# Optimization experiments

Hardware: AMD Instinct MI355X
Metric: run time of the kernel (lower is better)

Reference implementation:

```python
import jax, jax.numpy as jnp
import numpy as np

COMMITMENT_COST = 0.25


def setup_inputs() -> dict:
    key = jax.random.key(0)
    k1, k2 = jax.random.split(key)
    x = jax.random.normal(k1, (32, 1024, 512), dtype=jnp.float32)
    codebook = jax.random.normal(k2, (8192, 512), dtype=jnp.float32)
    return {"x": x, "codebook": codebook}


def reference(x, codebook):
    D = codebook.shape[1]
    flat = x.reshape(-1, D)                                   # [N, D]
    # squared L2 distances: ||f||^2 + ||c||^2 - 2 f c^T
    distances = (
        jnp.sum(flat * flat, axis=1, keepdims=True)
        + jnp.sum(codebook * codebook, axis=1)
        - 2.0 * jnp.matmul(flat, codebook.T)                   # [N, K]
    )
    encoding_indices = jnp.argmin(distances, axis=1)           # [N]
    quantized = codebook[encoding_indices].reshape(x.shape)    # [.., D]
    commitment_loss = COMMITMENT_COST * jnp.mean(
        (jax.lax.stop_gradient(quantized) - x) ** 2
    )
    # straight-through estimator
    quantized_st = x + jax.lax.stop_gradient(quantized - x)
    return (quantized_st, commitment_loss)
```

## Files before the change

### kernel.cpp

```cpp
#include <hip/hip_runtime.h>
#include <stdint.h>

#define N_TOT 32768
#define DDIM  512
#define KCB   8192
#define NSPLIT 4
#define COLS_SPLIT (KCB / NSPLIT)
#define BN 256
#define BC 256
#define BKD 64
#define NTILES (COLS_SPLIT / BC)
#define NSTEPS (NTILES * 8)
#define MARGIN 0.15f

#define RB3 32
#define RP3 32
#define RSLOTS (RGRID3 / RP3)
#define RGRID3 2048

typedef _Float16 half8 __attribute__((ext_vector_type(8)));
typedef float    floatx4 __attribute__((ext_vector_type(4)));

typedef const __attribute__((address_space(1))) unsigned int* gas_ptr;
typedef __attribute__((address_space(3))) unsigned int* las_ptr;
__device__ __forceinline__ void gld_lds16(void* l, const void* g) {
    __builtin_amdgcn_global_load_lds((gas_ptr)g, (las_ptr)l, 16, 0, 0);
}

__device__ __forceinline__ unsigned long long shfl_xor_u64(unsigned long long v, int m) {
    unsigned int lo = (unsigned int)v, hi = (unsigned int)(v >> 32);
    lo = __shfl_xor(lo, m, 64);
    hi = __shfl_xor(hi, m, 64);
    return ((unsigned long long)hi << 32) | lo;
}

__global__ __launch_bounds__(256) void convert_x_kernel(
    const float* __restrict__ x, _Float16* __restrict__ xh) {
    size_t i = ((size_t)blockIdx.x * 256 + threadIdx.x) * 8;
    float4 v0 = *(const float4*)(x + i);
    float4 v1 = *(const float4*)(x + i + 4);
    half8 h;
    h[0] = (_Float16)v0.x; h[1] = (_Float16)v0.y; h[2] = (_Float16)v0.z; h[3] = (_Float16)v0.w;
    h[4] = (_Float16)v1.x; h[5] = (_Float16)v1.y; h[6] = (_Float16)v1.z; h[7] = (_Float16)v1.w;
    *(half8*)(xh + i) = h;
}

__global__ __launch_bounds__(256) void convert_cb_kernel(
    const float* __restrict__ cb, _Float16* __restrict__ cbh, float* __restrict__ cnorm) {
    int row = blockIdx.x * 4 + (threadIdx.x >> 6);
    int lane = threadIdx.x & 63;
    const float* src = cb + (size_t)row * DDIM + lane * 8;
    float4 v0 = *(const float4*)src;
    float4 v1 = *(const float4*)(src + 4);
    half8 h;
    h[0] = (_Float16)v0.x; h[1] = (_Float16)v0.y; h[2] = (_Float16)v0.z; h[3] = (_Float16)v0.w;
    h[4] = (_Float16)v1.x; h[5] = (_Float16)v1.y; h[6] = (_Float16)v1.z; h[7] = (_Float16)v1.w;
    *(half8*)(cbh + (size_t)row * DDIM + lane * 8) = h;
    float s = v0.x*v0.x + v0.y*v0.y + v0.z*v0.z + v0.w*v0.w
            + v1.x*v1.x + v1.y*v1.y + v1.z*v1.z + v1.w*v1.w;
#pragma unroll
    for (int off = 32; off > 0; off >>= 1) s += __shfl_down(s, off, 64);
    if (lane == 0) cnorm[row] = s;
}

__global__ __launch_bounds__(512, 2) void gemm_argmin_kernel(
    const _Float16* __restrict__ xh, const _Float16* __restrict__ cbh,
    const float* __restrict__ cnorm,
    float* __restrict__ sb1, int* __restrict__ si1, float* __restrict__ sb2) {

    __shared__ __align__(16) _Float16 smem[65536];
    char* smemb = (char*)smem;

    const int tid = threadIdx.x;
    const int wave = tid >> 6;
    const int lane = tid & 63;
    const int rowPart = wave >> 1;
    const int colPart = wave & 1;
    const int l15 = lane & 15;
    const int quad = lane >> 4;

    const int orig = blockIdx.x;
    const int wg = (orig & 7) * 64 + (orig >> 3);
    const int bx = wg & 127;
    const int by = wg >> 7;
    const int row0 = bx * BN;
    const int colBase = by * COLS_SPLIT;

    int voff[4];
#pragma unroll
    for (int r = 0; r < 4; ++r) {
        int c = wave * 256 + r * 64 + lane;
        int ar = c >> 3;
        int q  = (c & 7) ^ (ar & 7);
        voff[r] = (ar << 9) + q * 8;
    }
    const _Float16* aptr = xh + ((size_t)row0 << 9);
    const _Float16* bptr = cbh + ((size_t)colBase << 9);

    int aaddr[4], baddr[8];
#pragma unroll
    for (int i = 0; i < 4; ++i) {
        int rr = rowPart * 64 + i * 16 + l15;
        int qa = quad ^ (rr & 7);
        aaddr[i] = rr * 128 + qa * 16;
    }
#pragma unroll
    for (int j = 0; j < 8; ++j) {
        int cc = colPart * 128 + j * 16 + l15;
        int qb = quad ^ (cc & 7);
        baddr[j] = 32768 + cc * 128 + qb * 16;
    }

    float b1[16], b2[16];
    int   i1[16];
#pragma unroll
    for (int s = 0; s < 16; ++s) { b1[s] = 3.402823466e38f; b2[s] = 3.402823466e38f; i1[s] = 0; }

#define STAGE(st) do {                                                          \
        _Float16* Asb = smem + ((st) & 1) * 32768;                              \
        _Float16* Bsb = Asb + 16384;                                            \
        const int boffu = ((st) >> 3) << 17;          \
        const int d0v   = ((st) & 7) * BKD;                                     \
        _Pragma("unroll")                                                       \
        for (int r = 0; r < 4; ++r) {                                           \
            gld_lds16(Asb + (wave * 256 + r * 64) * 8,                          \
                      aptr + d0v + voff[r]);                                    \
            gld_lds16(Bsb + (wave * 256 + r * 64) * 8,                          \
                      bptr + boffu + d0v + voff[r]);                            \
        }                                                                       \
    } while (0)

    floatx4 acc[4][8];
#pragma unroll
    for (int i = 0; i < 4; ++i)
#pragma unroll
        for (int j = 0; j < 8; ++j)
            acc[i][j] = (floatx4){0.f, 0.f, 0.f, 0.f};

    STAGE(0);
    STAGE(1);

    for (int s = 0; s < NSTEPS; ++s) {
        if (s + 1 < NSTEPS) {
            asm volatile("s_waitcnt vmcnt(8)" ::: "memory");
        } else {
            asm volatile("s_waitcnt vmcnt(0)" ::: "memory");
        }
        __builtin_amdgcn_sched_barrier(0);
        __builtin_amdgcn_s_barrier();
        __builtin_amdgcn_sched_barrier(0);

        const char* Ab = smemb + (s & 1) * 65536;
        __builtin_amdgcn_s_setprio(1);
#pragma unroll
        for (int kh = 0; kh < 2; ++kh) {
            half8 af[4], bf[8];
#pragma unroll
            for (int i = 0; i < 4; ++i)
                af[i] = *(const half8*)(Ab + (aaddr[i] ^ (kh << 6)));
#pragma unroll
            for (int j = 0; j < 8; ++j)
                bf[j] = *(const half8*)(Ab + (baddr[j] ^ (kh << 6)));
#pragma unroll
            for (int i = 0; i < 4; ++i)
#pragma unroll
                for (int j = 0; j < 8; ++j)
                    acc[i][j] = __builtin_amdgcn_mfma_f32_16x16x32_f16(
                        af[i], bf[j], acc[i][j], 0, 0, 0);
        }
        __builtin_amdgcn_s_setprio(0);

        if ((s & 7) == 7) {
            const int col0 = colBase + (s >> 3) * BC;
#pragma unroll
            for (int j = 0; j < 8; ++j) {
                int col = col0 + colPart * 128 + j * 16 + l15;
                float cn = cnorm[col];
#pragma unroll
                for (int i = 0; i < 4; ++i) {
#pragma unroll
                    for (int r = 0; r < 4; ++r) {
                        float sc = fmaf(-2.0f, acc[i][j][r], cn);
                        int slot = i * 4 + r;
                        if (sc < b1[slot]) { b2[slot] = b1[slot]; b1[slot] = sc; i1[slot] = col; }
                        else if (sc < b2[slot]) b2[slot] = sc;
                    }
                }
            }
#pragma unroll
            for (int i = 0; i < 4; ++i)
#pragma unroll
                for (int j = 0; j < 8; ++j)
                    acc[i][j] = (floatx4){0.f, 0.f, 0.f, 0.f};
        }

        __builtin_amdgcn_s_barrier();
        __builtin_amdgcn_sched_barrier(0);
        if (s + 2 < NSTEPS) {
            STAGE(s + 2);
        }
    }
#undef STAGE

    __syncthreads();

#pragma unroll
    for (int m = 1; m < 16; m <<= 1) {
#pragma unroll
        for (int s = 0; s < 16; ++s) {
            float ob1 = __shfl_xor(b1[s], m, 64);
            float ob2 = __shfl_xor(b2[s], m, 64);
            int   oi1 = __shfl_xor(i1[s], m, 64);
            if (ob1 < b1[s] || (ob1 == b1[s] && oi1 < i1[s])) {
                b2[s] = fminf(b1[s], ob2);
                b1[s] = ob1; i1[s] = oi1;
            } else {
                b2[s] = fminf(b2[s], ob1);
            }
        }
    }

    float* mb1 = (float*)smem;
    float* mb2 = mb1 + 512;
    int*   mi1 = (int*)(mb2 + 512);
    if (l15 == 0) {
#pragma unroll
        for (int s = 0; s < 16; ++s) {
            int row = rowPart * 64 + (s >> 2) * 16 + quad * 4 + (s & 3);
            mb1[colPart * 256 + row] = b1[s];
            mb2[colPart * 256 + row] = b2[s];
            mi1[colPart * 256 + row] = i1[s];
        }
    }
    __syncthreads();
    if (tid < 256) {
        float a1 = mb1[tid], a2 = mb2[tid]; int ai = mi1[tid];
        float c1 = mb1[256 + tid], c2 = mb2[256 + tid]; int ci = mi1[256 + tid];
        float r1, r2; int ri;
        if (c1 < a1 || (c1 == a1 && ci < ai)) { r1 = c1; ri = ci; r2 = fminf(a1, c2); }
        else { r1 = a1; ri = ai; r2 = fminf(a2, c1); }
        size_t o = (size_t)by * N_TOT + row0 + tid;
        sb1[o] = r1; si1[o] = ri; sb2[o] = r2;
    }
}

__global__ __launch_bounds__(256) void merge_kernel(
    const float* __restrict__ sb1, const int* __restrict__ si1, const float* __restrict__ sb2,
    int* __restrict__ indices, int* __restrict__ flags,
    int* __restrict__ list, int* __restrict__ count,
    unsigned long long* __restrict__ result) {
    int n = blockIdx.x * 256 + threadIdx.x;
    float b1 = sb1[n]; int i1 = si1[n]; float b2 = sb2[n];
#pragma unroll
    for (int s = 1; s < NSPLIT; ++s) {
        float ob1 = sb1[(size_t)s * N_TOT + n];
        int   oi1 = si1[(size_t)s * N_TOT + n];
        float ob2 = sb2[(size_t)s * N_TOT + n];
        if (ob1 < b1 || (ob1 == b1 && oi1 < i1)) { b2 = fminf(b1, ob2); b1 = ob1; i1 = oi1; }
        else b2 = fminf(b2, ob1);
    }
    indices[n] = i1;
    result[n] = 0xFFFFFFFFFFFFFFFFull;
    int f = (b2 - b1 < MARGIN) ? 1 : 0;
    flags[n] = f;
    if (f) { int pos = atomicAdd(count, 1); list[pos] = n; }
}

__global__ __launch_bounds__(256) void repair3_kernel(
    const float* __restrict__ x, const float* __restrict__ cb,
    const float* __restrict__ cnorm, const int* __restrict__ list,
    const int* __restrict__ count, unsigned long long* __restrict__ result) {
    __shared__ __align__(16) float xs[RB3][512];
    __shared__ unsigned long long red[RB3][4];
    const int tid = threadIdx.x;
    const int lane = tid & 63;
    const int wv = tid >> 6;
    const int part = blockIdx.x & (RP3 - 1);
    const int slot0 = blockIdx.x >> 5;
    const int cnt = *count;
    const int nbatch = (cnt + RB3 - 1) / RB3;
    const int k = part * 256 + tid;
    const float cn = cnorm[k];
    const float* crow = cb + (size_t)k * 512;

    for (int batch = slot0; batch < nbatch; batch += RSLOTS) {
        const int rb = min(RB3, cnt - batch * RB3);
        __syncthreads();
        for (int t = tid; t < rb * 128; t += 256) {
            int b = t >> 7, d4 = t & 127;
            int n = list[batch * RB3 + b];
            ((float4*)xs[b])[d4] = ((const float4*)(x + ((size_t)n << 9)))[d4];
        }
        __syncthreads();

        float d0[RB3], d1[RB3], d2[RB3], d3[RB3];
#pragma unroll
        for (int b = 0; b < RB3; ++b) { d0[b] = 0.f; d1[b] = 0.f; d2[b] = 0.f; d3[b] = 0.f; }

        for (int t = 0; t < 512; t += 16) {
            float4 c0 = *(const float4*)(crow + t);
            float4 c1 = *(const float4*)(crow + t + 4);
            float4 c2 = *(const float4*)(crow + t + 8);
            float4 c3 = *(const float4*)(crow + t + 12);
#pragma unroll
            for (int b = 0; b < RB3; ++b) {
                float4 x0 = *(const float4*)&xs[b][t];
                float4 x1 = *(const float4*)&xs[b][t + 4];
                float4 x2 = *(const float4*)&xs[b][t + 8];
                float4 x3 = *(const float4*)&xs[b][t + 12];
                d0[b] = fmaf(c0.x, x0.x, d0[b]);  d0[b] = fmaf(c0.y, x0.y, d0[b]);
                d0[b] = fmaf(c0.z, x0.z, d0[b]);  d0[b] = fmaf(c0.w, x0.w, d0[b]);
                d1[b] = fmaf(c1.x, x1.x, d1[b]);  d1[b] = fmaf(c1.y, x1.y, d1[b]);
                d1[b] = fmaf(c1.z, x1.z, d1[b]);  d1[b] = fmaf(c1.w, x1.w, d1[b]);
                d2[b] = fmaf(c2.x, x2.x, d2[b]);  d2[b] = fmaf(c2.y, x2.y, d2[b]);
                d2[b] = fmaf(c2.z, x2.z, d2[b]);  d2[b] = fmaf(c2.w, x2.w, d2[b]);
                d3[b] = fmaf(c3.x, x3.x, d3[b]);  d3[b] = fmaf(c3.y, x3.y, d3[b]);
                d3[b] = fmaf(c3.z, x3.z, d3[b]);  d3[b] = fmaf(c3.w, x3.w, d3[b]);
            }
        }

#pragma unroll
        for (int b = 0; b < RB3; ++b) {
            float s = cn - 2.f * ((d0[b] + d1[b]) + (d2[b] + d3[b]));
            unsigned int sb = __float_as_uint(s);
            sb = (sb & 0x80000000u) ? ~sb : (sb | 0x80000000u);
            unsigned long long p = ((unsigned long long)sb << 32) | (unsigned int)k;
#pragma unroll
            for (int m = 32; m > 0; m >>= 1) {
                unsigned long long o = shfl_xor_u64(p, m);
                if (o < p) p = o;
            }
            if (lane == 0) red[b][wv] = p;
        }
        __syncthreads();
        if (tid < RB3) {
            unsigned long long p = red[tid][0];
            if (red[tid][1] < p) p = red[tid][1];
            if (red[tid][2] < p) p = red[tid][2];
            if (red[tid][3] < p) p = red[tid][3];
            if (tid < rb) {
                int n = list[batch * RB3 + tid];
                atomicMin(&result[n], p);
            }
        }
    }
}

__global__ __launch_bounds__(256) void fixup_kernel(
    const int* __restrict__ flags, const unsigned long long* __restrict__ result,
    int* __restrict__ indices) {
    int n = blockIdx.x * 256 + threadIdx.x;
    if (flags[n]) indices[n] = (int)(result[n] & 0xFFFFFFFFu);
}

__global__ void cnorm_kernel(const float* __restrict__ cb, float* __restrict__ cnorm) {
    int wave = (blockIdx.x * blockDim.x + threadIdx.x) >> 6;
    int lane = threadIdx.x & 63;
    if (wave >= KCB) return;
    const float* row = cb + (size_t)wave * DDIM;
    float s = 0.f;
#pragma unroll
    for (int j = 0; j < DDIM / 64; ++j) { float v = row[lane + 64 * j]; s += v * v; }
#pragma unroll
    for (int off = 32; off > 0; off >>= 1) s += __shfl_down(s, off, 64);
    if (lane == 0) cnorm[wave] = s;
}

#define FBN 64
#define FBD 32
#define FLDA (FBN + 4)
__global__ __launch_bounds__(256) void argmin_fp32_kernel(
    const float* __restrict__ x, const float* __restrict__ cb,
    const float* __restrict__ cnorm, int* __restrict__ indices) {
    __shared__ float As[FBD][FLDA];
    __shared__ float Bs[FBD][FLDA];
    __shared__ float redv[FBN][16];
    __shared__ int   redi[FBN][16];
    const int tid = threadIdx.x;
    const int tx = tid & 15, ty = tid >> 4;
    const int row0 = blockIdx.x * FBN;
    float best[4]; int bidx[4];
#pragma unroll
    for (int i = 0; i < 4; ++i) { best[i] = 3.402823466e+38f; bidx[i] = KCB; }
    for (int k0 = 0; k0 < KCB; k0 += 64) {
        float acc[4][4] = {};
        for (int d0 = 0; d0 < DDIM; d0 += FBD) {
#pragma unroll
            for (int t = 0; t < 2; ++t) {
                int q = tid + t * 256, rr = q >> 3, dq = q & 7;
                float4 v = *(const float4*)(x + (size_t)(row0 + rr) * DDIM + d0 + dq * 4);
                As[dq*4+0][rr] = v.x; As[dq*4+1][rr] = v.y; As[dq*4+2][rr] = v.z; As[dq*4+3][rr] = v.w;
                float4 w = *(const float4*)(cb + (size_t)(k0 + rr) * DDIM + d0 + dq * 4);
                Bs[dq*4+0][rr] = w.x; Bs[dq*4+1][rr] = w.y; Bs[dq*4+2][rr] = w.z; Bs[dq*4+3][rr] = w.w;
            }
            __syncthreads();
#pragma unroll
            for (int d = 0; d < FBD; ++d) {
                float4 av = *(const float4*)&As[d][ty * 4];
                float4 bv = *(const float4*)&Bs[d][tx * 4];
                float a[4] = {av.x, av.y, av.z, av.w}, b[4] = {bv.x, bv.y, bv.z, bv.w};
#pragma unroll
                for (int i = 0; i < 4; ++i)
#pragma unroll
                    for (int j = 0; j < 4; ++j) acc[i][j] += a[i] * b[j];
            }
            __syncthreads();
        }
#pragma unroll
        for (int j = 0; j < 4; ++j) {
            int k = k0 + tx * 4 + j;
            float cn = cnorm[k];
#pragma unroll
            for (int i = 0; i < 4; ++i) {
                float s = cn - 2.0f * acc[i][j];
                if (s < best[i] || (s == best[i] && k < bidx[i])) { best[i] = s; bidx[i] = k; }
            }
        }
    }
#pragma unroll
    for (int i = 0; i < 4; ++i) { redv[ty*4+i][tx] = best[i]; redi[ty*4+i][tx] = bidx[i]; }
    __syncthreads();
    if (tid < FBN) {
        float bv = redv[tid][0]; int bi = redi[tid][0];
#pragma unroll
        for (int t = 1; t < 16; ++t) {
            float v = redv[tid][t]; int ii = redi[tid][t];
            if (v < bv || (v == bv && ii < bi)) { bv = v; bi = ii; }
        }
        indices[row0 + tid] = bi;
    }
}

__global__ __launch_bounds__(256) void output_kernel(
    const float* __restrict__ x, const float* __restrict__ cb,
    const int* __restrict__ indices, float* __restrict__ out,
    float* __restrict__ loss_acc) {
    size_t base = ((size_t)blockIdx.x * blockDim.x + threadIdx.x) * 16;
    int n = (int)(base >> 9);
    int d = (int)(base & 511);
    int idx = indices[n];
    const float* cr = cb + (size_t)idx * DDIM + d;
    const float* xr = x + base;
    float* orow = out + base;
    float lsum = 0.f;
#pragma unroll
    for (int t = 0; t < 4; ++t) {
        float4 q  = *(const float4*)(cr + t * 4);
        float4 xv = *(const float4*)(xr + t * 4);
        float dx0 = q.x - xv.x, dx1 = q.y - xv.y, dx2 = q.z - xv.z, dx3 = q.w - xv.w;
        float4 o;
        o.x = xv.x + dx0; o.y = xv.y + dx1; o.z = xv.z + dx2; o.w = xv.w + dx3;
        *(float4*)(orow + t * 4) = o;
        lsum += dx0*dx0 + dx1*dx1 + dx2*dx2 + dx3*dx3;
    }
#pragma unroll
    for (int off = 32; off > 0; off >>= 1) lsum += __shfl_down(lsum, off, 64);
    __shared__ float wsum[4];
    int lane = threadIdx.x & 63, wv = threadIdx.x >> 6;
    if (lane == 0) wsum[wv] = lsum;
    __syncthreads();
    if (threadIdx.x == 0) atomicAdd(loss_acc, wsum[0] + wsum[1] + wsum[2] + wsum[3]);
}

__global__ void finalize_kernel(const float* __restrict__ loss_acc, float* __restrict__ out_loss) {
    *out_loss = (*loss_acc) * (0.25f / (float)((size_t)N_TOT * DDIM));
}

extern "C" void kernel_launch(void* const* d_in, const int* in_sizes, int n_in,
                              void* d_out, int out_size, void* d_ws, size_t ws_size,
                              hipStream_t stream) {
    const float* x  = (const float*)d_in[0];
    const float* cb = (const float*)d_in[1];
    float* out = (float*)d_out;

    char* ws = (char*)d_ws;
    float* loss_acc = (float*)ws;
    int*   count    = (int*)(ws + 8);
    int*   indices  = (int*)(ws + 256);
    int*   flags    = (int*)(ws + 256 + 131072);
    float* cnorm    = (float*)(ws + 256 + 2 * 131072);
    int*   list     = (int*)(ws + 256 + 2 * 131072 + 32768);
    unsigned long long* result =
        (unsigned long long*)(ws + 256 + 3 * 131072 + 32768);
    size_t off = 256 + 3 * 131072 + 32768 + 262144;
    _Float16* xh  = (_Float16*)(ws + off);
    _Float16* cbh = (_Float16*)(ws + off + (size_t)N_TOT * DDIM * 2);
    size_t soff = off + (size_t)N_TOT * DDIM * 2 + (size_t)KCB * DDIM * 2;
    float* sb1 = (float*)(ws + soff);
    int*   si1 = (int*)(ws + soff + (size_t)NSPLIT * N_TOT * 4);
    float* sb2 = (float*)(ws + soff + (size_t)NSPLIT * N_TOT * 8);
    size_t need = soff + (size_t)NSPLIT * N_TOT * 12;

    hipMemsetAsync(ws, 0, 16, stream);
    if (ws_size >= need) {
        convert_x_kernel<<<(N_TOT * DDIM) / (256 * 8), 256, 0, stream>>>(x, xh);
        convert_cb_kernel<<<KCB / 4, 256, 0, stream>>>(cb, cbh, cnorm);
        gemm_argmin_kernel<<<(N_TOT / BN) * NSPLIT, 512, 0, stream>>>(
            xh, cbh, cnorm, sb1, si1, sb2);
        merge_kernel<<<N_TOT / 256, 256, 0, stream>>>(sb1, si1, sb2, indices, flags,
                                                      list, count, result);
        repair3_kernel<<<RGRID3, 256, 0, stream>>>(x, cb, cnorm, list, count, result);
        fixup_kernel<<<N_TOT / 256, 256, 0, stream>>>(flags, result, indices);
    } else {
        cnorm_kernel<<<KCB / 4, 256, 0, stream>>>(cb, cnorm);
        argmin_fp32_kernel<<<N_TOT / FBN, 256, 0, stream>>>(x, cb, cnorm, indices);
    }
    output_kernel<<<((size_t)N_TOT * DDIM) / (256 * 16), 256, 0, stream>>>(
        x, cb, indices, out, loss_acc);
    finalize_kernel<<<1, 1, 0, stream>>>(loss_acc, out + (size_t)N_TOT * DDIM);
}
```

Baseline: 836.2 us.

## Use 16-wave workgroups with smaller per-wave tiles and per-tile argmin reduction

The GEMM-argmin kernel moves from 8 to 16 waves per workgroup, so each wave computes a 64x64 sub-tile instead of 64x128. Accumulator registers are halved, and the running top-2 state shrinks from 16 slots per lane to one. The cross-lane shuffle reduction now runs every tile instead of once at the end. This is meant to cut register pressure and raise occupancy or latency hiding, at the cost of more shuffles and compares in the epilogue. Each wave also does fewer MFMAs per LDS fragment load, so the ratio of LDS reads to MFMA work goes up.

```diff
diff --git a/kernel.cpp b/kernel.cpp
--- a/kernel.cpp
+++ b/kernel.cpp
@@ -12,6 +12,7 @@
 #define NTILES (COLS_SPLIT / BC)
 #define NSTEPS (NTILES * 8)
 #define MARGIN 0.15f
+#define FLTMAX 3.402823466e38f
 
 #define RB3 32
 #define RP3 32
@@ -63,7 +64,7 @@
     if (lane == 0) cnorm[row] = s;
 }
 
-__global__ __launch_bounds__(512, 2) void gemm_argmin_kernel(
+__global__ __launch_bounds__(1024, 4) void gemm_argmin_kernel(
     const _Float16* __restrict__ xh, const _Float16* __restrict__ cbh,
     const float* __restrict__ cnorm,
     float* __restrict__ sb1, int* __restrict__ si1, float* __restrict__ sb2) {
@@ -74,8 +75,8 @@
     const int tid = threadIdx.x;
     const int wave = tid >> 6;
     const int lane = tid & 63;
-    const int rowPart = wave >> 1;
-    const int colPart = wave & 1;
+    const int rowPart = wave >> 2;
+    const int colPart = wave & 3;
     const int l15 = lane & 15;
     const int quad = lane >> 4;
 
@@ -86,10 +87,10 @@
     const int row0 = bx * BN;
     const int colBase = by * COLS_SPLIT;
 
-    int voff[4];
-#pragma unroll
-    for (int r = 0; r < 4; ++r) {
-        int c = wave * 256 + r * 64 + lane;
+    int voff[2];
+#pragma unroll
+    for (int r = 0; r < 2; ++r) {
+        int c = r * 1024 + wave * 64 + lane;
         int ar = c >> 3;
         int q  = (c & 7) ^ (ar & 7);
         voff[r] = (ar << 9) + q * 8;
@@ -97,24 +98,17 @@
     const _Float16* aptr = xh + ((size_t)row0 << 9);
     const _Float16* bptr = cbh + ((size_t)colBase << 9);
 
-    int aaddr[4], baddr[8];
+    int aaddr[4], baddr[4];
 #pragma unroll
     for (int i = 0; i < 4; ++i) {
         int rr = rowPart * 64 + i * 16 + l15;
-        int qa = quad ^ (rr & 7);
-        aaddr[i] = rr * 128 + qa * 16;
-    }
-#pragma unroll
-    for (int j = 0; j < 8; ++j) {
-        int cc = colPart * 128 + j * 16 + l15;
-        int qb = quad ^ (cc & 7);
-        baddr[j] = 32768 + cc * 128 + qb * 16;
-    }
-
-    float b1[16], b2[16];
-    int   i1[16];
-#pragma unroll
-    for (int s = 0; s < 16; ++s) { b1[s] = 3.402823466e38f; b2[s] = 3.402823466e38f; i1[s] = 0; }
+        aaddr[i] = rr * 128 + (quad ^ (rr & 7)) * 16;
+        int cc = colPart * 64 + i * 16 + l15;
+        baddr[i] = 32768 + cc * 128 + (quad ^ (cc & 7)) * 16;
+    }
+
+    float rb1 = FLTMAX, rb2 = FLTMAX;
+    int   ri  = 0;
 
 #define STAGE(st) do {                                                          \
         _Float16* Asb = smem + ((st) & 1) * 32768;                              \
@@ -122,19 +116,19 @@
         const int boffu = ((st) >> 3) << 17;          \
         const int d0v   = ((st) & 7) * BKD;                                     \
         _Pragma("unroll")                                                       \
-        for (int r = 0; r < 4; ++r) {                                           \
-            gld_lds16(Asb + (wave * 256 + r * 64) * 8,                          \
+        for (int r = 0; r < 2; ++r) {                                           \
+            gld_lds16(Asb + r * 8192 + (wave * 64 + lane) * 8,                  \
                       aptr + d0v + voff[r]);                                    \
-            gld_lds16(Bsb + (wave * 256 + r * 64) * 8,                          \
+            gld_lds16(Bsb + r * 8192 + (wave * 64 + lane) * 8,                  \
                       bptr + boffu + d0v + voff[r]);                            \
         }                                                                       \
     } while (0)
 
-    floatx4 acc[4][8];
+    floatx4 acc[4][4];
 #pragma unroll
     for (int i = 0; i < 4; ++i)
 #pragma unroll
-        for (int j = 0; j < 8; ++j)
+        for (int j = 0; j < 4; ++j)
             acc[i][j] = (floatx4){0.f, 0.f, 0.f, 0.f};
 
     STAGE(0);
@@ -142,7 +136,7 @@
 
     for (int s = 0; s < NSTEPS; ++s) {
         if (s + 1 < NSTEPS) {
-            asm volatile("s_waitcnt vmcnt(8)" ::: "memory");
+            asm volatile("s_waitcnt vmcnt(4)" ::: "memory");
         } else {
             asm volatile("s_waitcnt vmcnt(0)" ::: "memory");
         }
@@ -154,44 +148,67 @@
         __builtin_amdgcn_s_setprio(1);
 #pragma unroll
         for (int kh = 0; kh < 2; ++kh) {
-            half8 af[4], bf[8];
+            half8 af[4], bf[4];
 #pragma unroll
             for (int i = 0; i < 4; ++i)
                 af[i] = *(const half8*)(Ab + (aaddr[i] ^ (kh << 6)));
 #pragma unroll
-            for (int j = 0; j < 8; ++j)
+            for (int j = 0; j < 4; ++j)
                 bf[j] = *(const half8*)(Ab + (baddr[j] ^ (kh << 6)));
 #pragma unroll
             for (int i = 0; i < 4; ++i)
 #pragma unroll
-                for (int j = 0; j < 8; ++j)
+                for (int j = 0; j < 4; ++j)
                     acc[i][j] = __builtin_amdgcn_mfma_f32_16x16x32_f16(
                         af[i], bf[j], acc[i][j], 0, 0, 0);
         }
         __builtin_amdgcn_s_setprio(0);
 
         if ((s & 7) == 7) {
-            const int col0 = colBase + (s >> 3) * BC;
-#pragma unroll
-            for (int j = 0; j < 8; ++j) {
-                int col = col0 + colPart * 128 + j * 16 + l15;
-                float cn = cnorm[col];
-#pragma unroll
-                for (int i = 0; i < 4; ++i) {
+            const int col0 = colBase + (s >> 3) * BC + colPart * 64;
+#pragma unroll
+            for (int i = 0; i < 4; ++i) {
+                float t1[4], t2[4]; int ti[4];
+#pragma unroll
+                for (int r = 0; r < 4; ++r) { t1[r] = FLTMAX; t2[r] = FLTMAX; ti[r] = 0; }
+#pragma unroll
+                for (int j = 0; j < 4; ++j) {
+                    int col = col0 + j * 16 + l15;
+                    float cn = cnorm[col];
 #pragma unroll
                     for (int r = 0; r < 4; ++r) {
                         float sc = fmaf(-2.0f, acc[i][j][r], cn);
-                        int slot = i * 4 + r;
-                        if (sc < b1[slot]) { b2[slot] = b1[slot]; b1[slot] = sc; i1[slot] = col; }
-                        else if (sc < b2[slot]) b2[slot] = sc;
+                        if (sc < t1[r]) { t2[r] = t1[r]; t1[r] = sc; ti[r] = col; }
+                        else if (sc < t2[r]) t2[r] = sc;
+                    }
+                    acc[i][j] = (floatx4){0.f, 0.f, 0.f, 0.f};
+                }
+#pragma unroll
+                for (int m = 1; m < 16; m <<= 1) {
+#pragma unroll
+                    for (int r = 0; r < 4; ++r) {
+                        float o1 = __shfl_xor(t1[r], m, 64);
+                        float o2 = __shfl_xor(t2[r], m, 64);
+                        int   oi = __shfl_xor(ti[r], m, 64);
+                        if (o1 < t1[r] || (o1 == t1[r] && oi < ti[r])) {
+                            t2[r] = fminf(t1[r], o2);
+                            t1[r] = o1; ti[r] = oi;
+                        } else {
+                            t2[r] = fminf(t2[r], o1);
+                        }
                     }
                 }
-            }
-#pragma unroll
-            for (int i = 0; i < 4; ++i)
-#pragma unroll
-                for (int j = 0; j < 8; ++j)
-                    acc[i][j] = (floatx4){0.f, 0.f, 0.f, 0.f};
+#pragma unroll
+                for (int r = 0; r < 4; ++r) {
+                    if (l15 == i * 4 + r) {
+                        if (t1[r] < rb1 || (t1[r] == rb1 && ti[r] < ri)) {
+                            rb2 = fminf(rb1, t2[r]); rb1 = t1[r]; ri = ti[r];
+                        } else {
+                            rb2 = fminf(rb2, t1[r]);
+                        }
+                    }
+                }
+            }
         }
 
         __builtin_amdgcn_s_barrier();
@@ -204,43 +221,26 @@
 
     __syncthreads();
 
-#pragma unroll
-    for (int m = 1; m < 16; m <<= 1) {
-#pragma unroll
-        for (int s = 0; s < 16; ++s) {
-            float ob1 = __shfl_xor(b1[s], m, 64);
-            float ob2 = __shfl_xor(b2[s], m, 64);
-            int   oi1 = __shfl_xor(i1[s], m, 64);
-            if (ob1 < b1[s] || (ob1 == b1[s] && oi1 < i1[s])) {
-                b2[s] = fminf(b1[s], ob2);
-                b1[s] = ob1; i1[s] = oi1;
-            } else {
-                b2[s] = fminf(b2[s], ob1);
-            }
-        }
-    }
-
     float* mb1 = (float*)smem;
-    float* mb2 = mb1 + 512;
-    int*   mi1 = (int*)(mb2 + 512);
-    if (l15 == 0) {
-#pragma unroll
-        for (int s = 0; s < 16; ++s) {
-            int row = rowPart * 64 + (s >> 2) * 16 + quad * 4 + (s & 3);
-            mb1[colPart * 256 + row] = b1[s];
-            mb2[colPart * 256 + row] = b2[s];
-            mi1[colPart * 256 + row] = i1[s];
-        }
+    float* mb2 = mb1 + 1024;
+    int*   mi1 = (int*)(mb2 + 1024);
+    {
+        int row = rowPart * 64 + (l15 >> 2) * 16 + quad * 4 + (l15 & 3);
+        mb1[colPart * 256 + row] = rb1;
+        mb2[colPart * 256 + row] = rb2;
+        mi1[colPart * 256 + row] = ri;
     }
     __syncthreads();
     if (tid < 256) {
-        float a1 = mb1[tid], a2 = mb2[tid]; int ai = mi1[tid];
-        float c1 = mb1[256 + tid], c2 = mb2[256 + tid]; int ci = mi1[256 + tid];
-        float r1, r2; int ri;
-        if (c1 < a1 || (c1 == a1 && ci < ai)) { r1 = c1; ri = ci; r2 = fminf(a1, c2); }
-        else { r1 = a1; ri = ai; r2 = fminf(a2, c1); }
+        float b1v = mb1[tid], b2v = mb2[tid]; int iv = mi1[tid];
+#pragma unroll
+        for (int p = 1; p < 4; ++p) {
+            float c1 = mb1[p * 256 + tid], c2 = mb2[p * 256 + tid]; int ci = mi1[p * 256 + tid];
+            if (c1 < b1v || (c1 == b1v && ci < iv)) { b2v = fminf(b1v, c2); b1v = c1; iv = ci; }
+            else b2v = fminf(b2v, c1);
+        }
         size_t o = (size_t)by * N_TOT + row0 + tid;
-        sb1[o] = r1; si1[o] = ri; sb2[o] = r2;
+        sb1[o] = b1v; si1[o] = iv; sb2[o] = b2v;
     }
 }
 
@@ -495,7 +495,7 @@
     if (ws_size >= need) {
         convert_x_kernel<<<(N_TOT * DDIM) / (256 * 8), 256, 0, stream>>>(x, xh);
         convert_cb_kernel<<<KCB / 4, 256, 0, stream>>>(cb, cbh, cnorm);
-        gemm_argmin_kernel<<<(N_TOT / BN) * NSPLIT, 512, 0, stream>>>(
+        gemm_argmin_kernel<<<(N_TOT / BN) * NSPLIT, 1024, 0, stream>>>(
             xh, cbh, cnorm, sb1, si1, sb2);
         merge_kernel<<<N_TOT / 256, 256, 0, stream>>>(sb1, si1, sb2, indices, flags,
                                                       list, count, result);
```

Result: no change. 828.5 us (-0.9%).
